# Optimization experiments

Measured on AMD Instinct MI355X. Metric: run time of the kernel, lower is better.

The kernel has to match this reference:

```python
import jax, jax.numpy as jnp
import numpy as np

C = 256
NUM_HEADS = 4
GROUPS = 8
EPS = 1e-5


def setup_inputs() -> dict:
    key = jax.random.key(0)
    ks = jax.random.split(key, 8)
    N, H, W = 4, 64, 64
    x = jax.random.normal(ks[0], (N, C, H, W), dtype=jnp.float32)
    mask = jnp.ones((N, 1, H, W), dtype=jnp.float32)
    norm_w = jax.random.normal(ks[1], (C,), dtype=jnp.float32) * 0.02 + 1.0
    norm_b = jax.random.normal(ks[2], (C,), dtype=jnp.float32) * 0.02
    qkv_w = jax.random.normal(ks[3], (3 * C, C), dtype=jnp.float32) * (1.0 / np.sqrt(C))
    qkv_b = jax.random.normal(ks[4], (3 * C,), dtype=jnp.float32) * 0.02
    proj_w = jax.random.normal(ks[5], (C, C), dtype=jnp.float32) * (1.0 / np.sqrt(C))
    proj_b = jax.random.normal(ks[6], (C,), dtype=jnp.float32) * 0.02
    return {"x": x, "mask": mask, "norm_w": norm_w, "norm_b": norm_b,
            "qkv_w": qkv_w, "qkv_b": qkv_b, "proj_w": proj_w, "proj_b": proj_b}


def _group_norm(x, w, b):
    # x: [N, C, H, W]; normalize within GROUPS groups over (C//G, H, W)
    N, Cc, H, W = x.shape
    xg = x.reshape(N, GROUPS, Cc // GROUPS, H, W)
    mean = xg.mean(axis=(2, 3, 4), keepdims=True)
    var = xg.var(axis=(2, 3, 4), keepdims=True)
    xg = (xg - mean) * jax.lax.rsqrt(var + EPS)
    x = xg.reshape(N, Cc, H, W)
    return x * w[None, :, None, None] + b[None, :, None, None]


def reference(x, mask, norm_w, norm_b, qkv_w, qkv_b, proj_w, proj_b):
    N, Cc, H, W = x.shape
    h = NUM_HEADS
    hd = Cc // h  # head dim
    x_norm = _group_norm(x, norm_w, norm_b)
    # 1x1 conv == channel matmul: [N, 3C, H, W]
    qkv = jnp.einsum('nchw,oc->nohw', x_norm, qkv_w) + qkv_b[None, :, None, None]
    q, k, v = jnp.split(qkv, 3, axis=1)
    # n (h c) y x -> n h (y x) c
    def to_heads(t):
        return t.reshape(N, h, hd, H * W).transpose(0, 1, 3, 2)
    q, k, v = to_heads(q), to_heads(k), to_heads(v)
    scale = hd ** (-0.5)
    scores = jnp.einsum('nhic,nhjc->nhij', q, k) * scale  # [N,h,HW,HW]
    probs = jax.nn.softmax(scores, axis=-1)
    out = jnp.einsum('nhij,nhjc->nhic', probs, v)  # [N,h,HW,hd]
    # n h (y x) c -> n (h c) y x
    out = out.transpose(0, 1, 3, 2).reshape(N, Cc, H, W)
    out = jnp.einsum('nchw,oc->nohw', out, proj_w) + proj_b[None, :, None, None]
    y = (x + out) * mask[:, :1, :, :]  # broadcast over C (== repeat)
    return (y, mask)
```

## Files before the change

### kernel.cpp

```cpp
#include <hip/hip_runtime.h>

#define HW 4096
#define EPSV 1e-5f
#define SCL (0.125f * 1.44269504088896341f)

typedef unsigned short u16;
typedef unsigned int u32;
typedef __attribute__((ext_vector_type(8))) short short8;
typedef __attribute__((ext_vector_type(4))) short short4v;
typedef __attribute__((ext_vector_type(4))) float f32x4;

#define MFMA_K32(a, b, c) __builtin_amdgcn_mfma_f32_16x16x32_bf16((a), (b), (c), 0, 0, 0)
#if __has_builtin(__builtin_amdgcn_mfma_f32_16x16x16bf16_1k)
#define MFMA_K16(a, b, c) __builtin_amdgcn_mfma_f32_16x16x16bf16_1k((a), (b), (c), 0, 0, 0)
#elif __has_builtin(__builtin_amdgcn_mfma_f32_16x16x16_bf16)
#define MFMA_K16(a, b, c) __builtin_amdgcn_mfma_f32_16x16x16_bf16((a), (b), (c), 0, 0, 0)
#else
#define MFMA_K16(a, b, c) (c)
#endif

#define GLDS(g, l) __builtin_amdgcn_global_load_lds( \
    (const __attribute__((address_space(1))) u16*)(g), \
    (__attribute__((address_space(3))) u16*)(l), 16, 0, 0)

__device__ __forceinline__ u16 f2b(float f) {
    u32 u = __float_as_uint(f);
    u32 r = (u + 0x7FFFu + ((u >> 16) & 1u)) >> 16;
    return (u16)r;
}

__global__ __launch_bounds__(256) void gn_partial(const float* __restrict__ x, float* __restrict__ ps,
                                                  const float* __restrict__ mask, float* __restrict__ outm) {
    int bid = blockIdx.x;
    int t = threadIdx.x;
    if (bid < 16) {
        ((float4*)outm)[bid * 256 + t] = ((const float4*)mask)[bid * 256 + t];
    }
    const float4* base = (const float4*)x + (size_t)bid * 2048;
    float s = 0.f, sq = 0.f;
    for (int i = t; i < 2048; i += 256) {
        float4 v = base[i];
        s += v.x + v.y + v.z + v.w;
        sq += v.x * v.x + v.y * v.y + v.z * v.z + v.w * v.w;
    }
    __shared__ float rs[256], rq[256];
    rs[t] = s; rq[t] = sq;
    __syncthreads();
    for (int o = 128; o > 0; o >>= 1) {
        if (t < o) { rs[t] += rs[t + o]; rq[t] += rq[t + o]; }
        __syncthreads();
    }
    if (t == 0) { ps[2 * bid] = rs[0]; ps[2 * bid + 1] = rq[0]; }
}

__global__ __launch_bounds__(256) void prep(const float* __restrict__ ps, float* __restrict__ stats,
                                            const float* __restrict__ qkv_w, u16* __restrict__ Wqb,
                                            const float* __restrict__ proj_w, u16* __restrict__ Wpb) {
    int bid = blockIdx.x;
    int t = threadIdx.x;
    if (bid == 0) {
        if (t < 32) {
            float s = 0.f, sq = 0.f;
            for (int i = 0; i < 16; i++) {
                s += ps[2 * (t * 16 + i)];
                sq += ps[2 * (t * 16 + i) + 1];
            }
            float mean = s * (1.f / 131072.f);
            float var = sq * (1.f / 131072.f) - mean * mean;
            stats[t] = mean;
            stats[32 + t] = rsqrtf(var + EPSV);
        }
        return;
    }
    const float* src; u16* dst; int nscaled; int idx;
    if (bid <= 192) { src = qkv_w; dst = Wqb; nscaled = 256; idx = (bid - 1) * 256 + t; }
    else            { src = proj_w; dst = Wpb; nscaled = 0;   idx = (bid - 193) * 256 + t; }
    int row = idx >> 6;
    float sc = (row < nscaled) ? SCL : 1.0f;
    float4 v = *((const float4*)src + idx);
    u32 lo = (u32)f2b(v.x * sc) | ((u32)f2b(v.y * sc) << 16);
    u32 hi = (u32)f2b(v.z * sc) | ((u32)f2b(v.w * sc) << 16);
    uint2 o; o.x = lo; o.y = hi;
    *(uint2*)(dst + (size_t)idx * 4) = o;
}

__global__ __launch_bounds__(256) void gn_apply_t(const float* __restrict__ x, const float* __restrict__ w,
                                                  const float* __restrict__ b, const float* __restrict__ stats,
                                                  u16* __restrict__ xt) {
    __shared__ u16 Tt[64][72];
    int t = threadIdx.x;
    int p0 = blockIdx.x * 64;
    int c0 = blockIdx.y * 64;
    int n = blockIdx.z;
    int pc = (t & 15) * 4;
#pragma unroll
    for (int jj = 0; jj < 4; jj++) {
        int r = (t >> 4) + jj * 16;
        int c = c0 + r;
        int grp = n * 8 + (c >> 5);
        float mean = stats[grp], rstd = stats[32 + grp];
        float a = rstd * w[c];
        float bb = b[c] - mean * a;
        float4 v = *(const float4*)(x + ((size_t)n * 256 + c) * HW + p0 + pc);
        Tt[pc + 0][r] = f2b(v.x * a + bb);
        Tt[pc + 1][r] = f2b(v.y * a + bb);
        Tt[pc + 2][r] = f2b(v.z * a + bb);
        Tt[pc + 3][r] = f2b(v.w * a + bb);
    }
    __syncthreads();
    int p = t >> 2, ck = t & 3;
    short8 s0 = *(const short8*)&Tt[p][ck * 16];
    short8 s1 = *(const short8*)&Tt[p][ck * 16 + 8];
    u16* dst = xt + ((size_t)n * HW + p0 + p) * 256 + c0 + ck * 16;
    *(short8*)dst = s0;
    *(short8*)(dst + 8) = s1;
}

__global__ __launch_bounds__(256) void qkv_mfma(const u16* __restrict__ xt, const u16* __restrict__ Wb,
                                                const float* __restrict__ bq, u16* __restrict__ Qw,
                                                u16* __restrict__ Kw, u16* __restrict__ Vw) {
    __shared__ u16 Xs[64 * 256];
    int t = threadIdx.x;
    int w = t >> 6, lane = t & 63;
    int col = lane & 15, quad = lane >> 4;
    int p0 = blockIdx.x * 64;
    int oh = blockIdx.y;
    int n = blockIdx.z;

#pragma unroll
    for (int j = 0; j < 8; j++) {
        int rl = j * 2 + (lane >> 5);
        int row = w * 16 + rl;
        int slot = (lane & 31) ^ (rl & 7);
        GLDS(xt + ((size_t)n * HW + p0 + row) * 256 + slot * 8, Xs + (w * 16 + j * 2) * 256);
    }

    const u16* wrow = Wb + (size_t)(oh * 384 + w * 16 + col) * 256 + quad * 8;
    short8 A[8];
#pragma unroll
    for (int ks = 0; ks < 8; ks++) A[ks] = *(const short8*)(wrow + ks * 32);

    __syncthreads();

    int c7 = col & 7;
    for (int oi = 0; oi < 6; oi++) {
        int o0 = oh * 384 + oi * 64;
        short8 An[8];
        if (oi < 5) {
            const u16* wn = wrow + (size_t)(oi + 1) * 64 * 256;
#pragma unroll
            for (int ks = 0; ks < 8; ks++) An[ks] = *(const short8*)(wn + ks * 32);
        }

        f32x4 C[4];
#pragma unroll
        for (int pb = 0; pb < 4; pb++) C[pb] = (f32x4){0.f, 0.f, 0.f, 0.f};
#pragma unroll
        for (int pb = 0; pb < 4; pb++) {
            const u16* xr = Xs + (pb * 16 + col) * 256;
#pragma unroll
            for (int ks = 0; ks < 8; ks++) {
                int slot = (ks * 4 + quad) ^ c7;
                short8 Bf = *(const short8*)(xr + slot * 8);
                C[pb] = MFMA_K32(A[ks], Bf, C[pb]);
            }
        }

        int type = o0 >> 8;
        int h = (o0 >> 6) & 3;
        int nh = n * 4 + h;
        float sc = (type == 0) ? SCL : 1.0f;
        if (type == 2) {
#pragma unroll
            for (int rg = 0; rg < 4; rg++) {
                int d = w * 16 + quad * 4 + rg;
                float bias = bq[o0 + d];
                u16* vb = Vw + ((size_t)nh * 64 + d) * HW + p0 + col;
#pragma unroll
                for (int pb = 0; pb < 4; pb++)
                    vb[pb * 16] = f2b(C[pb][rg] + bias);
            }
        } else {
            u16* dst = (type == 0 ? Qw : Kw) + ((size_t)nh * HW + p0 + col) * 64 + w * 16 + quad * 4;
            float b0 = sc * bq[o0 + w * 16 + quad * 4 + 0];
            float b1 = sc * bq[o0 + w * 16 + quad * 4 + 1];
            float b2 = sc * bq[o0 + w * 16 + quad * 4 + 2];
            float b3 = sc * bq[o0 + w * 16 + quad * 4 + 3];
#pragma unroll
            for (int pb = 0; pb < 4; pb++) {
                uint2 o;
                o.x = (u32)f2b(C[pb][0] + b0) | ((u32)f2b(C[pb][1] + b1) << 16);
                o.y = (u32)f2b(C[pb][2] + b2) | ((u32)f2b(C[pb][3] + b3) << 16);
                *(uint2*)(dst + (size_t)(pb * 16) * 64) = o;
            }
        }
#pragma unroll
        for (int ks = 0; ks < 8; ks++) A[ks] = An[ks];
    }
}

__global__ __launch_bounds__(512, 4) void flash_mfma(const u16* __restrict__ Qw, const u16* __restrict__ Kw,
                                                     const u16* __restrict__ Vw, u16* __restrict__ attnT) {
    __shared__ u16 Ks[4][64 * 64];
    __shared__ u16 Vts[4][64 * 64];
    int t = threadIdx.x;
    int w = t >> 6, lane = t & 63;
    int half = w >> 2, wl = w & 3;
    int col = lane & 15, quad = lane >> 4;
    int q0 = blockIdx.x * 128;
    int nh = blockIdx.y;

    const u16* qp = Qw + ((size_t)nh * HW + q0 + wl * 32 + col) * 64 + quad * 8;
    short8 qa0 = *(const short8*)qp;
    short8 qa1 = *(const short8*)(qp + 32);
    short8 qc0 = *(const short8*)(qp + 1024);
    short8 qc1 = *(const short8*)(qp + 1024 + 32);

    f32x4 OaA[4], OaB[4];
#pragma unroll
    for (int db = 0; db < 4; db++) {
        OaA[db] = (f32x4){0.f, 0.f, 0.f, 0.f};
        OaB[db] = (f32x4){0.f, 0.f, 0.f, 0.f};
    }
    float lacA = 0.f, lacB = 0.f;

    const u16* kbase = Kw + (size_t)nh * HW * 64;
    const u16* vbase = Vw + (size_t)nh * 64 * HW;
    int lrK = lane >> 3;
    int ccK = lane & 7;
    size_t kSrc = (size_t)(wl * 8 + lrK) * 64 + (ccK ^ lrK) * 8;
    int jbase = half * 2048;

#define STAGE(jt_, b_) do { \
        int j0_ = jbase + (jt_) * 64; \
        _Pragma("unroll") \
        for (int s_ = 0; s_ < 2; s_++) \
            GLDS(kbase + (size_t)j0_ * 64 + kSrc + (size_t)(s_ * 32) * 64, &Ks[half * 2 + (b_)][(wl * 8 + s_ * 32) * 64]); \
        _Pragma("unroll") \
        for (int s_ = 0; s_ < 2; s_++) { \
            int d_ = wl * 8 + s_ * 32 + lrK; \
            GLDS(vbase + (size_t)d_ * HW + j0_ + ((ccK ^ lrK) * 8), &Vts[half * 2 + (b_)][(wl * 8 + s_ * 32) * 64]); \
        } \
    } while (0)

    STAGE(0, 0);
    STAGE(1, 1);

    int c7 = col & 7;
    for (int jt = 0; jt < 32; jt++) {
        int cur = jt & 1;
        if (jt < 31) { asm volatile("s_waitcnt vmcnt(4)" ::: "memory"); }
        else         { asm volatile("s_waitcnt vmcnt(0)" ::: "memory"); }
        __builtin_amdgcn_s_barrier();

        const u16* KsC = Ks[half * 2 + cur];
        const u16* VtC = Vts[half * 2 + cur];

        f32x4 sA[4], sB[4];
        __builtin_amdgcn_s_setprio(1);
#pragma unroll
        for (int jb = 0; jb < 4; jb++) {
            const u16* kr = KsC + (jb * 16 + col) * 64;
            short8 ka0 = *(const short8*)(kr + ((quad ^ c7) * 8));
            short8 ka1 = *(const short8*)(kr + (((quad + 4) ^ c7) * 8));
            f32x4 a = (f32x4){0.f, 0.f, 0.f, 0.f};
            a = MFMA_K32(ka0, qa0, a);
            a = MFMA_K32(ka1, qa1, a);
            sA[jb] = a;
            f32x4 b = (f32x4){0.f, 0.f, 0.f, 0.f};
            b = MFMA_K32(ka0, qc0, b);
            b = MFMA_K32(ka1, qc1, b);
            sB[jb] = b;
        }
        __builtin_amdgcn_s_setprio(0);

        short4v ptA[4], ptB[4];
#pragma unroll
        for (int jb = 0; jb < 4; jb++) {
            float ea0 = __builtin_amdgcn_exp2f(sA[jb][0]);
            float ea1 = __builtin_amdgcn_exp2f(sA[jb][1]);
            float ea2 = __builtin_amdgcn_exp2f(sA[jb][2]);
            float ea3 = __builtin_amdgcn_exp2f(sA[jb][3]);
            float eb0 = __builtin_amdgcn_exp2f(sB[jb][0]);
            float eb1 = __builtin_amdgcn_exp2f(sB[jb][1]);
            float eb2 = __builtin_amdgcn_exp2f(sB[jb][2]);
            float eb3 = __builtin_amdgcn_exp2f(sB[jb][3]);
            lacA += (ea0 + ea1) + (ea2 + ea3);
            lacB += (eb0 + eb1) + (eb2 + eb3);
            uint2 pa2, pb2;
            asm("v_cvt_pk_bf16_f32 %0, %1, %2" : "=v"(pa2.x) : "v"(ea0), "v"(ea1));
            asm("v_cvt_pk_bf16_f32 %0, %1, %2" : "=v"(pa2.y) : "v"(ea2), "v"(ea3));
            asm("v_cvt_pk_bf16_f32 %0, %1, %2" : "=v"(pb2.x) : "v"(eb0), "v"(eb1));
            asm("v_cvt_pk_bf16_f32 %0, %1, %2" : "=v"(pb2.y) : "v"(eb2), "v"(eb3));
            ptA[jb] = __builtin_bit_cast(short4v, pa2);
            ptB[jb] = __builtin_bit_cast(short4v, pb2);
        }

        __builtin_amdgcn_s_setprio(1);
#pragma unroll
        for (int db = 0; db < 4; db++) {
            const u16* vr = VtC + (db * 16 + col) * 64;
#pragma unroll
            for (int jb = 0; jb < 4; jb++) {
                int ch = jb * 2 + (quad >> 1);
                short4v va = *(const short4v*)(vr + ((ch ^ c7) * 8) + (quad & 1) * 4);
                OaA[db] = MFMA_K16(va, ptA[jb], OaA[db]);
                OaB[db] = MFMA_K16(va, ptB[jb], OaB[db]);
            }
        }
        __builtin_amdgcn_s_setprio(0);

        __builtin_amdgcn_s_barrier();
        if (jt < 30) STAGE(jt + 2, cur);
    }
#undef STAGE

    lacA += __shfl_xor(lacA, 16);
    lacB += __shfl_xor(lacB, 16);
    lacA += __shfl_xor(lacA, 32);
    lacB += __shfl_xor(lacB, 32);

    float* mO = (float*)&Ks[0][0];
    float* mL = (float*)&Vts[0][0];
    int widx = wl * 64 + lane;
    if (half == 1) {
#pragma unroll
        for (int db = 0; db < 4; db++) {
#pragma unroll
            for (int rg = 0; rg < 4; rg++) {
                mO[(db * 8 + rg) * 256 + widx] = OaA[db][rg];
                mO[(db * 8 + 4 + rg) * 256 + widx] = OaB[db][rg];
            }
        }
        mL[widx] = lacA;
        mL[256 + widx] = lacB;
    }
    __syncthreads();
    if (half == 0) {
        float lA = lacA + mL[widx];
        float lB = lacB + mL[256 + widx];
        float rlA = 1.0f / lA, rlB = 1.0f / lB;
        u16* abA = attnT + ((size_t)(nh >> 2) * HW + q0 + wl * 32 + col) * 256 + (nh & 3) * 64 + quad * 4;
        u16* abB = abA + 16 * 256;
#pragma unroll
        for (int db = 0; db < 4; db++) {
            float a0 = OaA[db][0] + mO[(db * 8 + 0) * 256 + widx];
            float a1 = OaA[db][1] + mO[(db * 8 + 1) * 256 + widx];
            float a2 = OaA[db][2] + mO[(db * 8 + 2) * 256 + widx];
            float a3 = OaA[db][3] + mO[(db * 8 + 3) * 256 + widx];
            float b0 = OaB[db][0] + mO[(db * 8 + 4) * 256 + widx];
            float b1 = OaB[db][1] + mO[(db * 8 + 5) * 256 + widx];
            float b2 = OaB[db][2] + mO[(db * 8 + 6) * 256 + widx];
            float b3 = OaB[db][3] + mO[(db * 8 + 7) * 256 + widx];
            uint2 oA, oB;
            oA.x = (u32)f2b(a0 * rlA) | ((u32)f2b(a1 * rlA) << 16);
            oA.y = (u32)f2b(a2 * rlA) | ((u32)f2b(a3 * rlA) << 16);
            oB.x = (u32)f2b(b0 * rlB) | ((u32)f2b(b1 * rlB) << 16);
            oB.y = (u32)f2b(b2 * rlB) | ((u32)f2b(b3 * rlB) << 16);
            *(uint2*)(abA + db * 16) = oA;
            *(uint2*)(abB + db * 16) = oB;
        }
    }
}

__global__ __launch_bounds__(256) void proj_mfma(const u16* __restrict__ attnT, const u16* __restrict__ Wpb,
                                                 const float* __restrict__ bp, const float* __restrict__ x,
                                                 const float* __restrict__ mask, float* __restrict__ out) {
    __shared__ u16 Xs[64 * 256];
    int t = threadIdx.x;
    int w = t >> 6, lane = t & 63;
    int col = lane & 15, quad = lane >> 4;
    int p0 = blockIdx.x * 64;
    int oh = blockIdx.y;
    int n = blockIdx.z;

#pragma unroll
    for (int j = 0; j < 8; j++) {
        int rl = j * 2 + (lane >> 5);
        int row = w * 16 + rl;
        int slot = (lane & 31) ^ (rl & 7);
        GLDS(attnT + ((size_t)n * HW + p0 + row) * 256 + slot * 8, Xs + (w * 16 + j * 2) * 256);
    }

    const u16* wrow = Wpb + (size_t)(oh * 128 + w * 16 + col) * 256 + quad * 8;
    short8 A[8];
#pragma unroll
    for (int ks = 0; ks < 8; ks++) A[ks] = *(const short8*)(wrow + ks * 32);

    __syncthreads();

    int c7 = col & 7;
    for (int oi = 0; oi < 2; oi++) {
        int o0 = oh * 128 + oi * 64;
        short8 An[8];
        if (oi < 1) {
            const u16* wn = wrow + (size_t)64 * 256;
#pragma unroll
            for (int ks = 0; ks < 8; ks++) An[ks] = *(const short8*)(wn + ks * 32);
        }

        f32x4 C[4];
#pragma unroll
        for (int pb = 0; pb < 4; pb++) C[pb] = (f32x4){0.f, 0.f, 0.f, 0.f};
#pragma unroll
        for (int pb = 0; pb < 4; pb++) {
            const u16* xr = Xs + (pb * 16 + col) * 256;
#pragma unroll
            for (int ks = 0; ks < 8; ks++) {
                int slot = (ks * 4 + quad) ^ c7;
                short8 Bf = *(const short8*)(xr + slot * 8);
                C[pb] = MFMA_K32(A[ks], Bf, C[pb]);
            }
        }

#pragma unroll
        for (int rg = 0; rg < 4; rg++) {
            int o = o0 + w * 16 + quad * 4 + rg;
            float bias = bp[o];
            const float* xb = x + ((size_t)n * 256 + o) * HW + p0 + col;
            float* ob = out + ((size_t)n * 256 + o) * HW + p0 + col;
            const float* mb = mask + (size_t)n * HW + p0 + col;
#pragma unroll
            for (int pb = 0; pb < 4; pb++) {
                float mv = mb[pb * 16];
                ob[pb * 16] = (xb[pb * 16] + C[pb][rg] + bias) * mv;
            }
        }
#pragma unroll
        for (int ks = 0; ks < 8; ks++) A[ks] = An[ks];
    }
}

extern "C" void kernel_launch(void* const* d_in, const int* in_sizes, int n_in,
                              void* d_out, int out_size, void* d_ws, size_t ws_size,
                              hipStream_t stream) {
    const float* x = (const float*)d_in[0];
    const float* mask = (const float*)d_in[1];
    const float* norm_w = (const float*)d_in[2];
    const float* norm_b = (const float*)d_in[3];
    const float* qkv_w = (const float*)d_in[4];
    const float* qkv_b = (const float*)d_in[5];
    const float* proj_w = (const float*)d_in[6];
    const float* proj_b = (const float*)d_in[7];
    float* out = (float*)d_out;

    float* ws = (float*)d_ws;
    float* stats = ws;
    float* pstats = ws + 64;
    u16* xt = (u16*)(ws + 2048);
    u16* Qw = xt + 4194304;
    u16* Kw = Qw + 4194304;
    u16* Vw = Kw + 4194304;
    u16* attnT = Vw + 4194304;
    u16* Wqb = attnT + 4194304;
    u16* Wpb = Wqb + 196608;

    gn_partial<<<512, 256, 0, stream>>>(x, pstats, mask, out + 4194304);
    prep<<<257, 256, 0, stream>>>(pstats, stats, qkv_w, Wqb, proj_w, Wpb);
    gn_apply_t<<<dim3(64, 4, 4), 256, 0, stream>>>(x, norm_w, norm_b, stats, xt);
    qkv_mfma<<<dim3(64, 2, 4), 256, 0, stream>>>(xt, Wqb, qkv_b, Qw, Kw, Vw);
    flash_mfma<<<dim3(32, 16), 512, 0, stream>>>(Qw, Kw, Vw, attnT);
    proj_mfma<<<dim3(64, 2, 4), 256, 0, stream>>>(attnT, Wpb, proj_b, x, mask, out);
}
```

Measured before the change: 199.7 us.

## Fuse group-norm apply into QKV GEMM and merge weight prep into stats kernel

Weight bf16 conversion moves into the group-norm partial-sum kernel, and the final stats reduction plus normalize/transpose is folded into the QKV GEMM kernel. That kernel now reads x directly, normalizes into shared memory, and computes all 768 output channels per block instead of splitting across two blocks. This removes two launches and the xt round trip through global memory. The cost is half as many QKV blocks (256 instead of 512), each doing twice the GEMM work, and each block redundantly recomputing group stats.

```diff
diff --git a/kernel.cpp b/kernel.cpp
--- a/kernel.cpp
+++ b/kernel.cpp
@@ -29,12 +29,26 @@
     return (u16)r;
 }
 
-__global__ __launch_bounds__(256) void gn_partial(const float* __restrict__ x, float* __restrict__ ps,
-                                                  const float* __restrict__ mask, float* __restrict__ outm) {
+__global__ __launch_bounds__(256) void gn_wprep(const float* __restrict__ x, float* __restrict__ ps,
+                                                const float* __restrict__ mask, float* __restrict__ outm,
+                                                const float* __restrict__ qkv_w, u16* __restrict__ Wqb,
+                                                const float* __restrict__ proj_w, u16* __restrict__ Wpb) {
     int bid = blockIdx.x;
     int t = threadIdx.x;
     if (bid < 16) {
         ((float4*)outm)[bid * 256 + t] = ((const float4*)mask)[bid * 256 + t];
+    }
+    if (bid < 256) {
+        const float* src; u16* dst; int nscaled; int idx;
+        if (bid < 192) { src = qkv_w; dst = Wqb; nscaled = 256; idx = bid * 256 + t; }
+        else           { src = proj_w; dst = Wpb; nscaled = 0;   idx = (bid - 192) * 256 + t; }
+        int row = idx >> 6;
+        float sc = (row < nscaled) ? SCL : 1.0f;
+        float4 v = *((const float4*)src + idx);
+        u32 lo = (u32)f2b(v.x * sc) | ((u32)f2b(v.y * sc) << 16);
+        u32 hi = (u32)f2b(v.z * sc) | ((u32)f2b(v.w * sc) << 16);
+        uint2 o; o.x = lo; o.y = hi;
+        *(uint2*)(dst + (size_t)idx * 4) = o;
     }
     const float4* base = (const float4*)x + (size_t)bid * 2048;
     float s = 0.f, sq = 0.f;
@@ -53,101 +67,70 @@
     if (t == 0) { ps[2 * bid] = rs[0]; ps[2 * bid + 1] = rq[0]; }
 }
 
-__global__ __launch_bounds__(256) void prep(const float* __restrict__ ps, float* __restrict__ stats,
-                                            const float* __restrict__ qkv_w, u16* __restrict__ Wqb,
-                                            const float* __restrict__ proj_w, u16* __restrict__ Wpb) {
-    int bid = blockIdx.x;
-    int t = threadIdx.x;
-    if (bid == 0) {
-        if (t < 32) {
-            float s = 0.f, sq = 0.f;
-            for (int i = 0; i < 16; i++) {
-                s += ps[2 * (t * 16 + i)];
-                sq += ps[2 * (t * 16 + i) + 1];
-            }
-            float mean = s * (1.f / 131072.f);
-            float var = sq * (1.f / 131072.f) - mean * mean;
-            stats[t] = mean;
-            stats[32 + t] = rsqrtf(var + EPSV);
-        }
-        return;
-    }
-    const float* src; u16* dst; int nscaled; int idx;
-    if (bid <= 192) { src = qkv_w; dst = Wqb; nscaled = 256; idx = (bid - 1) * 256 + t; }
-    else            { src = proj_w; dst = Wpb; nscaled = 0;   idx = (bid - 193) * 256 + t; }
-    int row = idx >> 6;
-    float sc = (row < nscaled) ? SCL : 1.0f;
-    float4 v = *((const float4*)src + idx);
-    u32 lo = (u32)f2b(v.x * sc) | ((u32)f2b(v.y * sc) << 16);
-    u32 hi = (u32)f2b(v.z * sc) | ((u32)f2b(v.w * sc) << 16);
-    uint2 o; o.x = lo; o.y = hi;
-    *(uint2*)(dst + (size_t)idx * 4) = o;
-}
-
-__global__ __launch_bounds__(256) void gn_apply_t(const float* __restrict__ x, const float* __restrict__ w,
-                                                  const float* __restrict__ b, const float* __restrict__ stats,
-                                                  u16* __restrict__ xt) {
+__global__ __launch_bounds__(256) void qkv_fused(const float* __restrict__ x, const float* __restrict__ ps,
+                                                 const float* __restrict__ nw, const float* __restrict__ nb,
+                                                 const u16* __restrict__ Wb, const float* __restrict__ bq,
+                                                 u16* __restrict__ Qw, u16* __restrict__ Kw, u16* __restrict__ Vw) {
+    __shared__ u16 Xs[64 * 256];
     __shared__ u16 Tt[64][72];
-    int t = threadIdx.x;
-    int p0 = blockIdx.x * 64;
-    int c0 = blockIdx.y * 64;
-    int n = blockIdx.z;
-    int pc = (t & 15) * 4;
-#pragma unroll
-    for (int jj = 0; jj < 4; jj++) {
-        int r = (t >> 4) + jj * 16;
-        int c = c0 + r;
-        int grp = n * 8 + (c >> 5);
-        float mean = stats[grp], rstd = stats[32 + grp];
-        float a = rstd * w[c];
-        float bb = b[c] - mean * a;
-        float4 v = *(const float4*)(x + ((size_t)n * 256 + c) * HW + p0 + pc);
-        Tt[pc + 0][r] = f2b(v.x * a + bb);
-        Tt[pc + 1][r] = f2b(v.y * a + bb);
-        Tt[pc + 2][r] = f2b(v.z * a + bb);
-        Tt[pc + 3][r] = f2b(v.w * a + bb);
-    }
-    __syncthreads();
-    int p = t >> 2, ck = t & 3;
-    short8 s0 = *(const short8*)&Tt[p][ck * 16];
-    short8 s1 = *(const short8*)&Tt[p][ck * 16 + 8];
-    u16* dst = xt + ((size_t)n * HW + p0 + p) * 256 + c0 + ck * 16;
-    *(short8*)dst = s0;
-    *(short8*)(dst + 8) = s1;
-}
-
-__global__ __launch_bounds__(256) void qkv_mfma(const u16* __restrict__ xt, const u16* __restrict__ Wb,
-                                                const float* __restrict__ bq, u16* __restrict__ Qw,
-                                                u16* __restrict__ Kw, u16* __restrict__ Vw) {
-    __shared__ u16 Xs[64 * 256];
+    __shared__ float gm[8], gr[8];
     int t = threadIdx.x;
     int w = t >> 6, lane = t & 63;
     int col = lane & 15, quad = lane >> 4;
     int p0 = blockIdx.x * 64;
-    int oh = blockIdx.y;
     int n = blockIdx.z;
 
-#pragma unroll
-    for (int j = 0; j < 8; j++) {
-        int rl = j * 2 + (lane >> 5);
-        int row = w * 16 + rl;
-        int slot = (lane & 31) ^ (rl & 7);
-        GLDS(xt + ((size_t)n * HW + p0 + row) * 256 + slot * 8, Xs + (w * 16 + j * 2) * 256);
-    }
-
-    const u16* wrow = Wb + (size_t)(oh * 384 + w * 16 + col) * 256 + quad * 8;
+    const u16* wrow = Wb + (size_t)(w * 16 + col) * 256 + quad * 8;
     short8 A[8];
 #pragma unroll
     for (int ks = 0; ks < 8; ks++) A[ks] = *(const short8*)(wrow + ks * 32);
 
+    if (t < 8) {
+        float s = 0.f, sq = 0.f;
+        for (int i = 0; i < 16; i++) {
+            s += ps[2 * ((n * 8 + t) * 16 + i)];
+            sq += ps[2 * ((n * 8 + t) * 16 + i) + 1];
+        }
+        float mean = s * (1.f / 131072.f);
+        float var = sq * (1.f / 131072.f) - mean * mean;
+        gm[t] = mean;
+        gr[t] = rsqrtf(var + EPSV);
+    }
     __syncthreads();
 
+    int pc = (t & 15) * 4;
+#pragma unroll
+    for (int cb = 0; cb < 4; cb++) {
+        int c0 = cb * 64;
+#pragma unroll
+        for (int jj = 0; jj < 4; jj++) {
+            int r = (t >> 4) + jj * 16;
+            int c = c0 + r;
+            int g = c >> 5;
+            float a = gr[g] * nw[c];
+            float bb = nb[c] - gm[g] * a;
+            float4 v = *(const float4*)(x + ((size_t)n * 256 + c) * HW + p0 + pc);
+            Tt[pc + 0][r] = f2b(v.x * a + bb);
+            Tt[pc + 1][r] = f2b(v.y * a + bb);
+            Tt[pc + 2][r] = f2b(v.z * a + bb);
+            Tt[pc + 3][r] = f2b(v.w * a + bb);
+        }
+        __syncthreads();
+        int p = t >> 2, ck = t & 3;
+        short8 s0 = *(const short8*)&Tt[p][ck * 16];
+        short8 s1 = *(const short8*)&Tt[p][ck * 16 + 8];
+        int ch0 = cb * 8 + ck * 2;
+        *(short8*)(Xs + p * 256 + ((ch0 ^ (p & 7)) * 8)) = s0;
+        *(short8*)(Xs + p * 256 + (((ch0 + 1) ^ (p & 7)) * 8)) = s1;
+        __syncthreads();
+    }
+
     int c7 = col & 7;
-    for (int oi = 0; oi < 6; oi++) {
-        int o0 = oh * 384 + oi * 64;
+    for (int ot = 0; ot < 12; ot++) {
+        int o0 = ot * 64;
         short8 An[8];
-        if (oi < 5) {
-            const u16* wn = wrow + (size_t)(oi + 1) * 64 * 256;
+        if (ot < 11) {
+            const u16* wn = wrow + (size_t)(o0 + 64) * 256;
 #pragma unroll
             for (int ks = 0; ks < 8; ks++) An[ks] = *(const short8*)(wn + ks * 32);
         }
@@ -445,7 +428,6 @@
     float* out = (float*)d_out;
 
     float* ws = (float*)d_ws;
-    float* stats = ws;
     float* pstats = ws + 64;
     u16* xt = (u16*)(ws + 2048);
     u16* Qw = xt + 4194304;
@@ -455,10 +437,8 @@
     u16* Wqb = attnT + 4194304;
     u16* Wpb = Wqb + 196608;
 
-    gn_partial<<<512, 256, 0, stream>>>(x, pstats, mask, out + 4194304);
-    prep<<<257, 256, 0, stream>>>(pstats, stats, qkv_w, Wqb, proj_w, Wpb);
-    gn_apply_t<<<dim3(64, 4, 4), 256, 0, stream>>>(x, norm_w, norm_b, stats, xt);
-    qkv_mfma<<<dim3(64, 2, 4), 256, 0, stream>>>(xt, Wqb, qkv_b, Qw, Kw, Vw);
+    gn_wprep<<<512, 256, 0, stream>>>(x, pstats, mask, out + 4194304, qkv_w, Wqb, proj_w, Wpb);
+    qkv_fused<<<dim3(64, 1, 4), 256, 0, stream>>>(x, pstats, norm_w, norm_b, Wqb, qkv_b, Qw, Kw, Vw);
     flash_mfma<<<dim3(32, 16), 512, 0, stream>>>(Qw, Kw, Vw, attnT);
     proj_mfma<<<dim3(64, 2, 4), 256, 0, stream>>>(attnT, Wpb, proj_b, x, mask, out);
 }
```

Measured after the change: 197.8 us. Within noise of the previous version (-0.9%).
